# Kernel optimization log

Measured on AMD Instinct MI355X. Metric: run time of the kernel, lower is better.

Reference implementation:

```python
import jax, jax.numpy as jnp
import numpy as np

B, L, E, H = 1, 2048, 1024, 16
D = E // H
SCALE = D ** -0.5


def rotary(x):
    # x: [b, h, L, d]; ESM-style rotary over the sequence axis
    d = x.shape[-1]
    inv_freq = 1.0 / (10000.0 ** (jnp.arange(0, d, 2, dtype=jnp.float32) / d))
    t = jnp.arange(x.shape[-2], dtype=jnp.float32)
    freqs = t[:, None] * inv_freq[None, :]            # [L, d/2]
    emb = jnp.concatenate([freqs, freqs], axis=-1)    # [L, d]
    cos, sin = jnp.cos(emb), jnp.sin(emb)
    x1, x2 = jnp.split(x, 2, axis=-1)
    rot = jnp.concatenate([-x2, x1], axis=-1)
    return x * cos + rot * sin


def setup_inputs() -> dict:
    key = jax.random.key(0)
    ks = jax.random.split(key, 12)
    s = 0.02
    return {
        "query": jax.random.normal(ks[0], (B, L, E), jnp.float32),
        "key_padding_mask": jnp.zeros((B, L), dtype=bool),
        "is_same_entity": jax.random.randint(ks[1], (B, L, L), 0, 2),
        "has_same_sequence": jax.random.randint(ks[2], (B, L, L), 0, 2),
        "Wq": jax.random.normal(ks[3], (E, E), jnp.float32) * s,
        "bq": jnp.zeros((E,), jnp.float32),
        "Wk": jax.random.normal(ks[4], (E, E), jnp.float32) * s,
        "bk": jnp.zeros((E,), jnp.float32),
        "Wv": jax.random.normal(ks[5], (E, E), jnp.float32) * s,
        "bv": jnp.zeros((E,), jnp.float32),
        "Wo": jax.random.normal(ks[6], (E, E), jnp.float32) * s,
        "bo": jnp.zeros((E,), jnp.float32),
        "ent_emb": jax.random.normal(ks[7], (2, H), jnp.float32) * s,
        "seq_emb": jax.random.normal(ks[8], (2, H), jnp.float32) * s,
    }


def reference(query, key_padding_mask, is_same_entity, has_same_sequence,
              Wq, bq, Wk, bk, Wv, bv, Wo, bo, ent_emb, seq_emb):
    b, l, e = query.shape
    h, d = H, e // H

    def proj(W, bias):
        y = jnp.einsum('ble,fe->blf', query, W) + bias
        return y.reshape(b, l, h, d).transpose(0, 2, 1, 3)  # [b,h,L,d]

    q = proj(Wq, bq) * SCALE
    k = proj(Wk, bk)
    v = proj(Wv, bv)

    # pre-rotary (raw) attention weights
    attn_raw = jnp.einsum('bhid,bhjd->bhij', q, k)
    q_r, k_r = rotary(q), rotary(k)
    attn = jnp.einsum('bhid,bhjd->bhij', q_r, k_r)

    # blend: use rotary weights within same sequence, mean-shifted raw elsewhere
    hss = has_same_sequence.astype(bool)[:, None, :, :]  # [b,1,L,L]
    attn_diff = jax.lax.stop_gradient(jnp.mean(attn - attn_raw, axis=(2, 3)))  # [b,h]
    attn_raw = attn_raw + attn_diff[:, :, None, None]
    w = jnp.where(hss, attn, attn_raw)

    # learned entity/sequence positional bias
    pos = ent_emb[is_same_entity] + seq_emb[has_same_sequence]  # [b,L,L,h]
    w = w + jnp.transpose(pos, (0, 3, 1, 2))

    w = jnp.where(key_padding_mask[:, None, None, :], -jnp.inf, w)
    a = jax.nn.softmax(w, axis=-1)

    o = jnp.einsum('bhij,bhjd->bhid', a, v)
    o = o.transpose(0, 2, 1, 3).reshape(b, l, e)
    return jnp.einsum('ble,fe->blf', o, Wo) + bo
```

## Files before the change

### kernel.cpp

```cpp
#include <hip/hip_runtime.h>
#include <math.h>

constexpr int L = 2048;
constexpr int E = 1024;
constexpr int H = 16;
constexpr int D = 64;
constexpr float ATT_SCALE = 0.125f;

typedef __attribute__((ext_vector_type(8))) short short8;
typedef __attribute__((ext_vector_type(4))) float f32x4;

__device__ inline unsigned short cvt_bf16(float x) {
  unsigned int u = __builtin_bit_cast(unsigned int, x);
  unsigned int r = u + 0x7fffu + ((u >> 16) & 1u);
  return (unsigned short)(r >> 16);
}

__device__ inline short8 ld8(const unsigned short* p) {
  return *reinterpret_cast<const short8*>(p);
}

__global__ __launch_bounds__(256) void rope_table_k(float* __restrict__ cos_t,
                                                    float* __restrict__ sin_t) {
  int idx = blockIdx.x * 256 + threadIdx.x;
  if (idx >= L * 32) return;
  int l = idx >> 5, m = idx & 31;
  double invf = exp(-(double)m * (log(10000.0) / 32.0));
  double ph = (double)l * invf;
  cos_t[idx] = (float)cos(ph);
  sin_t[idx] = (float)sin(ph);
}

__global__ __launch_bounds__(256) void cvt_bf16_k(const float* __restrict__ src,
                                                  unsigned short* __restrict__ dst,
                                                  int n8) {
  int i = blockIdx.x * 256 + threadIdx.x;
  if (i >= n8) return;
  const float4* s = (const float4*)src;
  float4 a = s[i * 2], b = s[i * 2 + 1];
  short8 o;
  o[0] = cvt_bf16(a.x); o[1] = cvt_bf16(a.y); o[2] = cvt_bf16(a.z); o[3] = cvt_bf16(a.w);
  o[4] = cvt_bf16(b.x); o[5] = cvt_bf16(b.y); o[6] = cvt_bf16(b.z); o[7] = cvt_bf16(b.w);
  *(short8*)&dst[(size_t)i * 8] = o;
}

__global__ __launch_bounds__(256) void mask_pack_k(const int* __restrict__ hss,
                                                   const int* __restrict__ ise,
                                                   unsigned char* __restrict__ mbf) {
  int idx = blockIdx.x * 256 + threadIdx.x;
  int i = idx >> 9;
  int rem = idx & 511;
  int jt = rem >> 4, lr = rem & 15;
  size_t rb = (size_t)i * 2048 + jt * 64 + lr;
  unsigned int out = 0;
#pragma unroll
  for (int c = 0; c < 4; ++c) {
    unsigned int hv = (unsigned)hss[rb + c * 16] & 1u;
    unsigned int ev = (unsigned)ise[rb + c * 16] & 1u;
    out |= (hv | (ev << 1)) << (8 * c);
  }
  *(unsigned int*)&mbf[(size_t)i * 2048 + jt * 64 + lr * 4] = out;
}

__global__ __launch_bounds__(256) void proj_mfma(
    const unsigned short* __restrict__ Xb, const unsigned short* __restrict__ Wb,
    const float* __restrict__ bias, float* __restrict__ Y, float scale, int mode) {
  int tid = threadIdx.x;
  int w = tid >> 6, lane = tid & 63, lr = lane & 15, lg = lane >> 4;
  int wm = w >> 1, wn = w & 1;
  int row0 = blockIdx.x * 128, col0 = blockIdx.y * 64;

  f32x4 acc[4][2];
#pragma unroll
  for (int m = 0; m < 4; ++m)
#pragma unroll
    for (int n = 0; n < 2; ++n) acc[m][n] = f32x4{0.f, 0.f, 0.f, 0.f};

  const unsigned short* xa[4];
  const unsigned short* wb[2];
#pragma unroll
  for (int m = 0; m < 4; ++m)
    xa[m] = Xb + (size_t)(row0 + wm * 64 + m * 16 + lr) * 1024 + lg * 8;
#pragma unroll
  for (int n = 0; n < 2; ++n)
    wb[n] = Wb + (size_t)(col0 + wn * 32 + n * 16 + lr) * 1024 + lg * 8;

  for (int k0 = 0; k0 < 1024; k0 += 64) {
    short8 a[4][2], b[2][2];
#pragma unroll
    for (int m = 0; m < 4; ++m) {
      a[m][0] = ld8(xa[m] + k0);
      a[m][1] = ld8(xa[m] + k0 + 32);
    }
#pragma unroll
    for (int n = 0; n < 2; ++n) {
      b[n][0] = ld8(wb[n] + k0);
      b[n][1] = ld8(wb[n] + k0 + 32);
    }
#pragma unroll
    for (int m = 0; m < 4; ++m)
#pragma unroll
      for (int n = 0; n < 2; ++n) {
        acc[m][n] = __builtin_amdgcn_mfma_f32_16x16x32_bf16(a[m][0], b[n][0], acc[m][n], 0, 0, 0);
        acc[m][n] = __builtin_amdgcn_mfma_f32_16x16x32_bf16(a[m][1], b[n][1], acc[m][n], 0, 0, 0);
      }
  }

#pragma unroll
  for (int m = 0; m < 4; ++m)
#pragma unroll
    for (int n = 0; n < 2; ++n) {
      int f = col0 + wn * 32 + n * 16 + lr;
      float bv = bias[f];
#pragma unroll
      for (int rr = 0; rr < 4; ++rr) {
        int l = row0 + wm * 64 + m * 16 + lg * 4 + rr;
        float val = (acc[m][n][rr] + bv) * scale;
        if (mode == 0) Y[((size_t)(f >> 6) * L + l) * 64 + (f & 63)] = val;
        else           Y[(size_t)l * 1024 + f] = val;
      }
    }
}

__global__ __launch_bounds__(256) void postproc_k(
    const float* __restrict__ q, const float* __restrict__ k,
    unsigned short* __restrict__ qb, unsigned short* __restrict__ qrb,
    unsigned short* __restrict__ kb, unsigned short* __restrict__ krb,
    const float* __restrict__ cos_t, const float* __restrict__ sin_t,
    float* __restrict__ sums) {
  int h = blockIdx.x;
  int lc = blockIdx.y;
  int t = threadIdx.x;
  int d = t & 63, lq = t >> 6;
  int m = d & 31;
  float sign = (d < 32) ? -1.0f : 1.0f;
  float sq = 0.f, sk = 0.f, sqr = 0.f, skr = 0.f;
#pragma unroll 4
  for (int i = 0; i < 16; ++i) {
    int l = lc * 64 + i * 4 + lq;
    size_t base = ((size_t)h * L + l) * 64 + d;
    float cv = cos_t[l * 32 + m], sv = sin_t[l * 32 + m];
    float qv = q[base];
    float qp = __shfl_xor(qv, 32);
    float qrv = qv * cv + sign * qp * sv;
    float kv = k[base];
    float kp = __shfl_xor(kv, 32);
    float krv = kv * cv + sign * kp * sv;
    qb[base] = cvt_bf16(qv);
    qrb[base] = cvt_bf16(qrv);
    kb[base] = cvt_bf16(kv);
    krb[base] = cvt_bf16(krv);
    sq += qv; sk += kv; sqr += qrv; skr += krv;
  }
  __shared__ float red[256];
  float vals[4] = {sq, sk, sqr, skr};
#pragma unroll
  for (int a = 0; a < 4; ++a) {
    red[t] = vals[a];
    __syncthreads();
    if (lq == 0) {
      float tot = red[d] + red[d + 64] + red[d + 128] + red[d + 192];
      atomicAdd(&sums[((size_t)a * H + h) * D + d], tot);
    }
    __syncthreads();
  }
}

__global__ __launch_bounds__(256) void vt_k(const float* __restrict__ v,
                                            unsigned short* __restrict__ vtb) {
  __shared__ float tile[64][65];
  int h = blockIdx.x, lt = blockIdx.y, t = threadIdx.x;
  int row = t >> 2, cq = (t & 3) * 16;
  const float* src = v + ((size_t)h * L + lt * 64 + row) * 64 + cq;
#pragma unroll
  for (int x = 0; x < 4; ++x) {
    float4 a = *(const float4*)&src[x * 4];
    tile[row][cq + x * 4 + 0] = a.x;
    tile[row][cq + x * 4 + 1] = a.y;
    tile[row][cq + x * 4 + 2] = a.z;
    tile[row][cq + x * 4 + 3] = a.w;
  }
  __syncthreads();
  int dcol = t >> 2, lq = (t & 3) * 16;
  short8 o0, o1;
#pragma unroll
  for (int x = 0; x < 8; ++x) o0[x] = cvt_bf16(tile[lq + x][dcol]);
#pragma unroll
  for (int x = 0; x < 8; ++x) o1[x] = cvt_bf16(tile[lq + 8 + x][dcol]);
  unsigned short* dst = vtb + ((size_t)h * 64 + dcol) * L + lt * 64 + lq;
  *(short8*)dst = o0;
  *(short8*)(dst + 8) = o1;
}

__global__ void diff_k(const float* __restrict__ sums, float* __restrict__ diffp) {
  int h = threadIdx.x;
  if (h < H) {
    const float* sq  = sums + (0 * H + h) * D;
    const float* sk  = sums + (1 * H + h) * D;
    const float* sqr = sums + (2 * H + h) * D;
    const float* skr = sums + (3 * H + h) * D;
    float a = 0.f, b = 0.f;
    for (int d = 0; d < D; ++d) { a += sqr[d] * skr[d]; b += sq[d] * sk[d]; }
    diffp[h] = (a - b) / ((float)L * (float)L);
  }
}

__global__ __launch_bounds__(256) void attn_mfma(
    const unsigned short* __restrict__ qb, const unsigned short* __restrict__ qrb,
    const unsigned short* __restrict__ kb, const unsigned short* __restrict__ krb,
    const unsigned short* __restrict__ vtb, const unsigned char* __restrict__ mbf,
    const float* __restrict__ diffp, const float* __restrict__ ent,
    const float* __restrict__ seq, unsigned short* __restrict__ ob) {
  __shared__ char p_s[8192];

  int bid = blockIdx.x;
  int xcd = bid & 7, g = bid >> 3;
  int h = xcd * 2 + (g >> 5);
  int it = g & 31;
  int i0 = it * 64;

  int tid = threadIdx.x;
  int w = tid >> 6, lane = tid & 63, lr = lane & 15, lg = lane >> 4;

  const size_t hb = (size_t)h * L * 64;
  const unsigned short* qh = qb + hb;
  const unsigned short* qrh = qrb + hb;
  const unsigned short* kh = kb + hb;
  const unsigned short* krh = krb + hb;
  const unsigned short* vth = vtb + hb;

  short8 aq[2], aqr[2];
  {
    size_t qbase = (size_t)(i0 + w * 16 + lr) * 64 + lg * 8;
    aq[0] = ld8(qh + qbase);
    aq[1] = ld8(qh + qbase + 32);
    aqr[0] = ld8(qrh + qbase);
    aqr[1] = ld8(qrh + qbase + 32);
  }

  float e0 = ent[h], de = ent[H + h] - e0;
  float s0b = seq[h], dsb = seq[H + h] - s0b;
  float base_b = e0 + s0b;
  float dh = diffp[h];

  float m_r[4], l_r[4];
  f32x4 oacc[4];
#pragma unroll
  for (int rr = 0; rr < 4; ++rr) { m_r[rr] = -INFINITY; l_r[rr] = 0.f; }
#pragma unroll
  for (int n = 0; n < 4; ++n) oacc[n] = f32x4{0.f, 0.f, 0.f, 0.f};

  int koff[4];
#pragma unroll
  for (int c = 0; c < 4; ++c) koff[c] = (c * 16 + lr) * 64 + lg * 8;
  size_t vtoff[4];
#pragma unroll
  for (int n = 0; n < 4; ++n) vtoff[n] = (size_t)(n * 16 + lr) * L + lg * 8;
  int prd0 = w * 2048 + lr * 128 + ((lg * 16) ^ ((lr & 7) << 4));
  int prd1 = w * 2048 + lr * 128 + ((64 + lg * 16) ^ ((lr & 7) << 4));
  size_t mrow0 = (size_t)(i0 + w * 16 + lg * 4) * 2048 + lr * 4;

  for (int jt = 0; jt < 32; ++jt) {
    int j0 = jt * 64;
    int jb = j0 * 64;

    f32x4 sraw[4], srot[4];
#pragma unroll
    for (int c = 0; c < 4; ++c) {
      sraw[c] = f32x4{0.f, 0.f, 0.f, 0.f};
      srot[c] = f32x4{0.f, 0.f, 0.f, 0.f};
    }
#pragma unroll
    for (int c = 0; c < 4; ++c) {
      short8 b0 = ld8(kh + jb + koff[c]);
      short8 b1 = ld8(kh + jb + koff[c] + 32);
      sraw[c] = __builtin_amdgcn_mfma_f32_16x16x32_bf16(aq[0], b0, sraw[c], 0, 0, 0);
      sraw[c] = __builtin_amdgcn_mfma_f32_16x16x32_bf16(aq[1], b1, sraw[c], 0, 0, 0);
      short8 r0 = ld8(krh + jb + koff[c]);
      short8 r1 = ld8(krh + jb + koff[c] + 32);
      srot[c] = __builtin_amdgcn_mfma_f32_16x16x32_bf16(aqr[0], r0, srot[c], 0, 0, 0);
      srot[c] = __builtin_amdgcn_mfma_f32_16x16x32_bf16(aqr[1], r1, srot[c], 0, 0, 0);
    }

    unsigned int mw[4];
#pragma unroll
    for (int rr = 0; rr < 4; ++rr)
      mw[rr] = *(const unsigned int*)(mbf + mrow0 + (size_t)rr * 2048 + j0);

#pragma unroll
    for (int rr = 0; rr < 4; ++rr) {
      float sv[4];
#pragma unroll
      for (int c = 0; c < 4; ++c) {
        unsigned int b = (mw[rr] >> (8 * c)) & 0xffu;
        float srv = sraw[c][rr] + dh;
        float sov = srot[c][rr];
        float s = ((b & 1) ? sov : srv) + base_b + ((b & 1) ? dsb : 0.f) + ((b & 2) ? de : 0.f);
        sv[c] = s;
      }
      float tmax = fmaxf(fmaxf(sv[0], sv[1]), fmaxf(sv[2], sv[3]));
#pragma unroll
      for (int off = 1; off <= 8; off <<= 1) tmax = fmaxf(tmax, __shfl_xor(tmax, off));
      float mnew = fmaxf(m_r[rr], tmax);
      float corr = __expf(m_r[rr] - mnew);
      float p[4];
      float psum = 0.f;
#pragma unroll
      for (int c = 0; c < 4; ++c) { p[c] = __expf(sv[c] - mnew); psum += p[c]; }
#pragma unroll
      for (int off = 1; off <= 8; off <<= 1) psum += __shfl_xor(psum, off);
      l_r[rr] = l_r[rr] * corr + psum;
      m_r[rr] = mnew;
#pragma unroll
      for (int n = 0; n < 4; ++n) oacc[n][rr] *= corr;
      int prow = lg * 4 + rr;
      int pb = w * 2048 + prow * 128;
      int sw = (prow & 7) << 4;
#pragma unroll
      for (int c = 0; c < 4; ++c)
        *(unsigned short*)(p_s + pb + (((c * 16 + lr) * 2) ^ sw)) = cvt_bf16(p[c]);
    }

    short8 pa0 = *(const short8*)(p_s + prd0);
    short8 pa1 = *(const short8*)(p_s + prd1);
#pragma unroll
    for (int n = 0; n < 4; ++n) {
      short8 v0 = ld8(vth + vtoff[n] + j0);
      short8 v1 = ld8(vth + vtoff[n] + j0 + 32);
      oacc[n] = __builtin_amdgcn_mfma_f32_16x16x32_bf16(pa0, v0, oacc[n], 0, 0, 0);
      oacc[n] = __builtin_amdgcn_mfma_f32_16x16x32_bf16(pa1, v1, oacc[n], 0, 0, 0);
    }
  }

#pragma unroll
  for (int rr = 0; rr < 4; ++rr) {
    float inv = 1.0f / l_r[rr];
    size_t orow = (size_t)(i0 + w * 16 + lg * 4 + rr) * 1024 + h * 64;
#pragma unroll
    for (int n = 0; n < 4; ++n)
      ob[orow + n * 16 + lr] = cvt_bf16(oacc[n][rr] * inv);
  }
}

extern "C" void kernel_launch(void* const* d_in, const int* in_sizes, int n_in,
                              void* d_out, int out_size, void* d_ws, size_t ws_size,
                              hipStream_t stream) {
  (void)in_sizes; (void)n_in; (void)out_size; (void)ws_size;
  const float* query = (const float*)d_in[0];
  const int* ise = (const int*)d_in[2];
  const int* hss = (const int*)d_in[3];
  const float* Wq = (const float*)d_in[4];
  const float* bq = (const float*)d_in[5];
  const float* Wk = (const float*)d_in[6];
  const float* bk = (const float*)d_in[7];
  const float* Wv = (const float*)d_in[8];
  const float* bv = (const float*)d_in[9];
  const float* Wo = (const float*)d_in[10];
  const float* bo = (const float*)d_in[11];
  const float* ent = (const float*)d_in[12];
  const float* seq = (const float*)d_in[13];
  float* out = (float*)d_out;

  const size_t MQ = (size_t)L * E;
  const size_t MW = (size_t)E * E;

  float* ws = (float*)d_ws;
  float* qf = ws;
  float* kf = ws + MQ;
  float* vf = ws + 2 * MQ;

  unsigned short* ub = (unsigned short*)(ws + 3 * MQ);
  unsigned short* xb  = ub;
  unsigned short* wqb = xb + MQ;
  unsigned short* wkb = wqb + MW;
  unsigned short* wvb = wkb + MW;
  unsigned short* wob = wvb + MW;
  unsigned short* qb2 = wob + MW;
  unsigned short* qrb = qb2 + MQ;
  unsigned short* kb2 = qrb + MQ;
  unsigned short* krb = kb2 + MQ;
  unsigned short* vtb = krb + MQ;
  unsigned short* obf = vtb + MQ;

  unsigned char* mbf = (unsigned char*)(obf + MQ);
  float* tail = (float*)(mbf + (size_t)L * L);
  float* cs = tail;
  float* sn = cs + (size_t)L * 32;
  float* sums = sn + (size_t)L * 32;
  float* diffp = sums + 4096;

  rope_table_k<<<256, 256, 0, stream>>>(cs, sn);

  cvt_bf16_k<<<(int)(MQ / 8 + 255) / 256, 256, 0, stream>>>(query, xb, (int)(MQ / 8));
  cvt_bf16_k<<<(int)(MW / 8 + 255) / 256, 256, 0, stream>>>(Wq, wqb, (int)(MW / 8));
  cvt_bf16_k<<<(int)(MW / 8 + 255) / 256, 256, 0, stream>>>(Wk, wkb, (int)(MW / 8));
  cvt_bf16_k<<<(int)(MW / 8 + 255) / 256, 256, 0, stream>>>(Wv, wvb, (int)(MW / 8));
  cvt_bf16_k<<<(int)(MW / 8 + 255) / 256, 256, 0, stream>>>(Wo, wob, (int)(MW / 8));

  mask_pack_k<<<4096, 256, 0, stream>>>(hss, ise, mbf);

  dim3 gp(16, 16);
  proj_mfma<<<gp, 256, 0, stream>>>(xb, wqb, bq, qf, ATT_SCALE, 0);
  proj_mfma<<<gp, 256, 0, stream>>>(xb, wkb, bk, kf, 1.0f, 0);
  proj_mfma<<<gp, 256, 0, stream>>>(xb, wvb, bv, vf, 1.0f, 0);

  hipMemsetAsync(sums, 0, 4096 * sizeof(float), stream);
  postproc_k<<<dim3(16, 32), 256, 0, stream>>>(qf, kf, qb2, qrb, kb2, krb, cs, sn, sums);
  vt_k<<<dim3(16, 32), 256, 0, stream>>>(vf, vtb);
  diff_k<<<1, 64, 0, stream>>>(sums, diffp);

  attn_mfma<<<512, 256, 0, stream>>>(qb2, qrb, kb2, krb, vtb, mbf, diffp, ent, seq, obf);

  proj_mfma<<<gp, 256, 0, stream>>>(obf, wob, bo, out, 1.0f, 1);
}
```

Baseline: 440.5 us.

## Merge bf16 conversions and QKV projections into single launches with smaller tiles

The five separate fp32-to-bf16 conversion launches become one kernel that picks its source by global index. The three Q/K/V projection GEMMs become one launch over a 3x grid, with the source selected per block. Both the QKV and output projections shrink their row tile from 128 to 64, giving more blocks (1536 and 512 instead of 256 each) to fill the GPU, and add a partial unroll of the k-loop. The aim is to cut launch overhead and improve occupancy, at the cost of less A/B reuse per block and more global load traffic.

Result: faster. 428.4 us (-2.7%).

```diff
diff --git a/kernel.cpp b/kernel.cpp
--- a/kernel.cpp
+++ b/kernel.cpp
@@ -15,7 +15,6 @@
   unsigned int r = u + 0x7fffu + ((u >> 16) & 1u);
   return (unsigned short)(r >> 16);
 }
-
 __device__ inline short8 ld8(const unsigned short* p) {
   return *reinterpret_cast<const short8*>(p);
 }
@@ -31,17 +30,24 @@
   sin_t[idx] = (float)sin(ph);
 }
 
-__global__ __launch_bounds__(256) void cvt_bf16_k(const float* __restrict__ src,
-                                                  unsigned short* __restrict__ dst,
-                                                  int n8) {
-  int i = blockIdx.x * 256 + threadIdx.x;
-  if (i >= n8) return;
-  const float4* s = (const float4*)src;
-  float4 a = s[i * 2], b = s[i * 2 + 1];
+__global__ __launch_bounds__(256) void cvt_all_k(
+    const float* __restrict__ q, const float* __restrict__ wq,
+    const float* __restrict__ wk, const float* __restrict__ wv,
+    const float* __restrict__ wo, unsigned short* __restrict__ dst) {
+  int idx = blockIdx.x * 256 + threadIdx.x;
+  const float* src;
+  int local;
+  if (idx < 262144)      { src = q;  local = idx; }
+  else if (idx < 393216) { src = wq; local = idx - 262144; }
+  else if (idx < 524288) { src = wk; local = idx - 393216; }
+  else if (idx < 655360) { src = wv; local = idx - 524288; }
+  else                   { src = wo; local = idx - 655360; }
+  const float4* s = (const float4*)src + (size_t)local * 2;
+  float4 a = s[0], b = s[1];
   short8 o;
   o[0] = cvt_bf16(a.x); o[1] = cvt_bf16(a.y); o[2] = cvt_bf16(a.z); o[3] = cvt_bf16(a.w);
   o[4] = cvt_bf16(b.x); o[5] = cvt_bf16(b.y); o[6] = cvt_bf16(b.z); o[7] = cvt_bf16(b.w);
-  *(short8*)&dst[(size_t)i * 8] = o;
+  *(short8*)&dst[(size_t)idx * 8] = o;
 }
 
 __global__ __launch_bounds__(256) void mask_pack_k(const int* __restrict__ hss,
@@ -62,43 +68,56 @@
   *(unsigned int*)&mbf[(size_t)i * 2048 + jt * 64 + lr * 4] = out;
 }
 
-__global__ __launch_bounds__(256) void proj_mfma(
-    const unsigned short* __restrict__ Xb, const unsigned short* __restrict__ Wb,
-    const float* __restrict__ bias, float* __restrict__ Y, float scale, int mode) {
+__global__ __launch_bounds__(256) void proj_qkv(
+    const unsigned short* __restrict__ Xb,
+    const unsigned short* __restrict__ wqb, const unsigned short* __restrict__ wkb,
+    const unsigned short* __restrict__ wvb,
+    const float* __restrict__ bq, const float* __restrict__ bk,
+    const float* __restrict__ bv,
+    float* __restrict__ qf, float* __restrict__ kf, float* __restrict__ vf) {
+  int by = blockIdx.y;
+  int sel = by >> 4;
+  int col0 = (by & 15) * 64;
+  int row0 = blockIdx.x * 64;
+  const unsigned short* Wb = (sel == 0) ? wqb : (sel == 1) ? wkb : wvb;
+  const float* bias = (sel == 0) ? bq : (sel == 1) ? bk : bv;
+  float scale = (sel == 0) ? ATT_SCALE : 1.0f;
+  float* Y = (sel == 0) ? qf : (sel == 1) ? kf : vf;
+
   int tid = threadIdx.x;
   int w = tid >> 6, lane = tid & 63, lr = lane & 15, lg = lane >> 4;
   int wm = w >> 1, wn = w & 1;
-  int row0 = blockIdx.x * 128, col0 = blockIdx.y * 64;
-
-  f32x4 acc[4][2];
-#pragma unroll
-  for (int m = 0; m < 4; ++m)
+
+  f32x4 acc[2][2];
+#pragma unroll
+  for (int m = 0; m < 2; ++m)
 #pragma unroll
     for (int n = 0; n < 2; ++n) acc[m][n] = f32x4{0.f, 0.f, 0.f, 0.f};
 
-  const unsigned short* xa[4];
-  const unsigned short* wb[2];
-#pragma unroll
-  for (int m = 0; m < 4; ++m)
-    xa[m] = Xb + (size_t)(row0 + wm * 64 + m * 16 + lr) * 1024 + lg * 8;
+  const unsigned short* xa[2];
+  const unsigned short* wb2[2];
+#pragma unroll
+  for (int m = 0; m < 2; ++m)
+    xa[m] = Xb + (size_t)(row0 + wm * 32 + m * 16 + lr) * 1024 + lg * 8;
 #pragma unroll
   for (int n = 0; n < 2; ++n)
-    wb[n] = Wb + (size_t)(col0 + wn * 32 + n * 16 + lr) * 1024 + lg * 8;
-
+    wb2[n] = Wb + (size_t)(col0 + wn * 32 + n * 16 + lr) * 1024 + lg * 8;
+
+#pragma unroll 2
   for (int k0 = 0; k0 < 1024; k0 += 64) {
-    short8 a[4][2], b[2][2];
-#pragma unroll
-    for (int m = 0; m < 4; ++m) {
+    short8 a[2][2], b[2][2];
+#pragma unroll
+    for (int m = 0; m < 2; ++m) {
       a[m][0] = ld8(xa[m] + k0);
       a[m][1] = ld8(xa[m] + k0 + 32);
     }
 #pragma unroll
     for (int n = 0; n < 2; ++n) {
-      b[n][0] = ld8(wb[n] + k0);
-      b[n][1] = ld8(wb[n] + k0 + 32);
-    }
-#pragma unroll
-    for (int m = 0; m < 4; ++m)
+      b[n][0] = ld8(wb2[n] + k0);
+      b[n][1] = ld8(wb2[n] + k0 + 32);
+    }
+#pragma unroll
+    for (int m = 0; m < 2; ++m)
 #pragma unroll
       for (int n = 0; n < 2; ++n) {
         acc[m][n] = __builtin_amdgcn_mfma_f32_16x16x32_bf16(a[m][0], b[n][0], acc[m][n], 0, 0, 0);
@@ -107,17 +126,75 @@
   }
 
 #pragma unroll
-  for (int m = 0; m < 4; ++m)
+  for (int m = 0; m < 2; ++m)
 #pragma unroll
     for (int n = 0; n < 2; ++n) {
       int f = col0 + wn * 32 + n * 16 + lr;
-      float bv = bias[f];
+      float bvv = bias[f];
 #pragma unroll
       for (int rr = 0; rr < 4; ++rr) {
-        int l = row0 + wm * 64 + m * 16 + lg * 4 + rr;
-        float val = (acc[m][n][rr] + bv) * scale;
-        if (mode == 0) Y[((size_t)(f >> 6) * L + l) * 64 + (f & 63)] = val;
-        else           Y[(size_t)l * 1024 + f] = val;
+        int row = row0 + wm * 32 + m * 16 + lg * 4 + rr;
+        Y[((size_t)(f >> 6) * L + row) * 64 + (f & 63)] = (acc[m][n][rr] + bvv) * scale;
+      }
+    }
+}
+
+__global__ __launch_bounds__(256) void proj_o(
+    const unsigned short* __restrict__ Xb, const unsigned short* __restrict__ Wb,
+    const float* __restrict__ bias, float* __restrict__ out) {
+  int col0 = blockIdx.y * 64;
+  int row0 = blockIdx.x * 64;
+  int tid = threadIdx.x;
+  int w = tid >> 6, lane = tid & 63, lr = lane & 15, lg = lane >> 4;
+  int wm = w >> 1, wn = w & 1;
+
+  f32x4 acc[2][2];
+#pragma unroll
+  for (int m = 0; m < 2; ++m)
+#pragma unroll
+    for (int n = 0; n < 2; ++n) acc[m][n] = f32x4{0.f, 0.f, 0.f, 0.f};
+
+  const unsigned short* xa[2];
+  const unsigned short* wb2[2];
+#pragma unroll
+  for (int m = 0; m < 2; ++m)
+    xa[m] = Xb + (size_t)(row0 + wm * 32 + m * 16 + lr) * 1024 + lg * 8;
+#pragma unroll
+  for (int n = 0; n < 2; ++n)
+    wb2[n] = Wb + (size_t)(col0 + wn * 32 + n * 16 + lr) * 1024 + lg * 8;
+
+#pragma unroll 2
+  for (int k0 = 0; k0 < 1024; k0 += 64) {
+    short8 a[2][2], b[2][2];
+#pragma unroll
+    for (int m = 0; m < 2; ++m) {
+      a[m][0] = ld8(xa[m] + k0);
+      a[m][1] = ld8(xa[m] + k0 + 32);
+    }
+#pragma unroll
+    for (int n = 0; n < 2; ++n) {
+      b[n][0] = ld8(wb2[n] + k0);
+      b[n][1] = ld8(wb2[n] + k0 + 32);
+    }
+#pragma unroll
+    for (int m = 0; m < 2; ++m)
+#pragma unroll
+      for (int n = 0; n < 2; ++n) {
+        acc[m][n] = __builtin_amdgcn_mfma_f32_16x16x32_bf16(a[m][0], b[n][0], acc[m][n], 0, 0, 0);
+        acc[m][n] = __builtin_amdgcn_mfma_f32_16x16x32_bf16(a[m][1], b[n][1], acc[m][n], 0, 0, 0);
+      }
+  }
+
+#pragma unroll
+  for (int m = 0; m < 2; ++m)
+#pragma unroll
+    for (int n = 0; n < 2; ++n) {
+      int f = col0 + wn * 32 + n * 16 + lr;
+      float bvv = bias[f];
+#pragma unroll
+      for (int rr = 0; rr < 4; ++rr) {
+        int row = row0 + wm * 32 + m * 16 + lg * 4 + rr;
+        out[(size_t)row * 1024 + f] = acc[m][n][rr] + bvv;
       }
     }
 }
@@ -369,8 +446,7 @@
   float* kf = ws + MQ;
   float* vf = ws + 2 * MQ;
 
-  unsigned short* ub = (unsigned short*)(ws + 3 * MQ);
-  unsigned short* xb  = ub;
+  unsigned short* xb  = (unsigned short*)(ws + 3 * MQ);
   unsigned short* wqb = xb + MQ;
   unsigned short* wkb = wqb + MW;
   unsigned short* wvb = wkb + MW;
@@ -390,19 +466,10 @@
   float* diffp = sums + 4096;
 
   rope_table_k<<<256, 256, 0, stream>>>(cs, sn);
-
-  cvt_bf16_k<<<(int)(MQ / 8 + 255) / 256, 256, 0, stream>>>(query, xb, (int)(MQ / 8));
-  cvt_bf16_k<<<(int)(MW / 8 + 255) / 256, 256, 0, stream>>>(Wq, wqb, (int)(MW / 8));
-  cvt_bf16_k<<<(int)(MW / 8 + 255) / 256, 256, 0, stream>>>(Wk, wkb, (int)(MW / 8));
-  cvt_bf16_k<<<(int)(MW / 8 + 255) / 256, 256, 0, stream>>>(Wv, wvb, (int)(MW / 8));
-  cvt_bf16_k<<<(int)(MW / 8 + 255) / 256, 256, 0, stream>>>(Wo, wob, (int)(MW / 8));
-
+  cvt_all_k<<<3072, 256, 0, stream>>>(query, Wq, Wk, Wv, Wo, xb);
   mask_pack_k<<<4096, 256, 0, stream>>>(hss, ise, mbf);
 
-  dim3 gp(16, 16);
-  proj_mfma<<<gp, 256, 0, stream>>>(xb, wqb, bq, qf, ATT_SCALE, 0);
-  proj_mfma<<<gp, 256, 0, stream>>>(xb, wkb, bk, kf, 1.0f, 0);
-  proj_mfma<<<gp, 256, 0, stream>>>(xb, wvb, bv, vf, 1.0f, 0);
+  proj_qkv<<<dim3(32, 48), 256, 0, stream>>>(xb, wqb, wkb, wvb, bq, bk, bv, qf, kf, vf);
 
   hipMemsetAsync(sums, 0, 4096 * sizeof(float), stream);
   postproc_k<<<dim3(16, 32), 256, 0, stream>>>(qf, kf, qb2, qrb, kb2, krb, cs, sn, sums);
@@ -411,5 +478,5 @@
 
   attn_mfma<<<512, 256, 0, stream>>>(qb2, qrb, kb2, krb, vtb, mbf, diffp, ent, seq, obf);
 
-  proj_mfma<<<gp, 256, 0, stream>>>(obf, wob, bo, out, 1.0f, 1);
-}
+  proj_o<<<dim3(32, 16), 256, 0, stream>>>(obf, wob, bo, out);
+}
```
